# Kernel tuning notes

Hardware: AMD Instinct MI355X
Metric: run time of the kernel (lower is better)

## Reference

```python
import jax, jax.numpy as jnp
import numpy as np
import math

E = 1024      # embed_dim
H = 16        # num_heads
D = E // H    # head_dim = 64 (power of two, padded_dim == head_dim)


def fwht(x):
    """Normalized fast Walsh-Hadamard transform on last dim (power of two)."""
    n = x.shape[-1]
    orig = x.shape
    x = x.reshape(-1, n)
    h = 1
    while h < n:  # log2(n) fixed butterfly stages
        x = x.reshape(-1, n // (2 * h), 2, h)
        a, b = x[:, :, 0, :], x[:, :, 1, :]
        x = jnp.stack([a + b, a - b], axis=2).reshape(-1, n)
        h *= 2
    return (x / math.sqrt(n)).reshape(orig)


def apply_transform(x, diag, alpha, bias):
    # x: [b, h, s, d]; gated FWHT-domain diagonal filter residual
    x_f = fwht(x) * diag
    x_inv = fwht(x_f)
    return x + alpha * x_inv + bias


def setup_inputs() -> dict:
    key = jax.random.key(0)
    ks = jax.random.split(key, 6)
    b, s = 2, 2048
    sc_in = 1.0 / math.sqrt(E)
    return {
        "x": jax.random.normal(ks[0], (b, s, E), jnp.float32),
        "mask": jnp.ones((b, s), jnp.int32),
        "Wqkv": jax.random.normal(ks[1], (E, 3 * E), jnp.float32) * sc_in,
        "bqkv": jnp.zeros((3 * E,), jnp.float32),
        "Wout": jax.random.normal(ks[2], (E, E), jnp.float32) * sc_in,
        "bout": jnp.zeros((E,), jnp.float32),
        "diag": jnp.ones((D,), jnp.float32) * 0.05,
        "alpha": jnp.float32(0.1),
        "bias_h": jnp.zeros((D,), jnp.float32),
    }


def reference(x, mask, Wqkv, bqkv, Wout, bout, diag, alpha, bias_h):
    b, s, _ = x.shape
    qkv = x @ Wqkv + bqkv                       # [b, s, 3E]
    q, k, v = jnp.split(qkv, 3, axis=-1)

    def to_heads(t):
        return t.reshape(b, s, H, D).transpose(0, 2, 1, 3)  # [b, h, s, d]

    qh, kh, vh = to_heads(q), to_heads(k), to_heads(v)
    qh = apply_transform(qh, diag, alpha, bias_h)
    kh = apply_transform(kh, diag, alpha, bias_h)

    scores = jnp.einsum('bhqd,bhkd->bhqk', qh, kh) / math.sqrt(D)
    scores = jnp.where(mask[:, None, None, :] == 0, -jnp.inf, scores)
    weights = jax.nn.softmax(scores, axis=-1)

    out = jnp.einsum('bhqk,bhkd->bhqd', weights, vh)
    out = out.transpose(0, 2, 1, 3).reshape(b, s, E)
    return out @ Wout + bout
```

## Files before the change

kernel.cpp:

```cpp
#include <hip/hip_runtime.h>
#include <hip/hip_bf16.h>
#include <cmath>

#define B_ 2
#define S_ 2048
#define E_ 1024
#define H_ 16
#define M_ (B_*S_)
#define N3_ (3*E_)

typedef unsigned short u16;
typedef unsigned int u32;
typedef __attribute__((ext_vector_type(8))) short bf16x8;
typedef __attribute__((ext_vector_type(8))) _Float16 f16x8;
typedef __attribute__((ext_vector_type(4))) float f32x4;

__device__ __forceinline__ float hw_exp2(float x) {
    return __builtin_amdgcn_exp2f(x);
}
__device__ __forceinline__ u16 cvt_bf(float x) {
    return __builtin_bit_cast(u16, __float2bfloat16(x));
}
__device__ __forceinline__ float bf2f(u16 h) {
    return __uint_as_float((u32)h << 16);
}
__device__ __forceinline__ u16 f2h(float x) {
    _Float16 h = (_Float16)x;
    return __builtin_bit_cast(u16, h);
}
__device__ __forceinline__ float h2f(u16 b) {
    return (float)__builtin_bit_cast(_Float16, b);
}
__device__ __forceinline__ void gld_lds16(const void* g, void* l) {
    __builtin_amdgcn_global_load_lds((const __attribute__((address_space(1))) void*)g,
                                     (__attribute__((address_space(3))) void*)l, 16, 0, 0);
}

template<bool F16>
__device__ __forceinline__ f32x4 mma16(bf16x8 a, bf16x8 b, f32x4 c) {
    if constexpr (F16)
        return __builtin_amdgcn_mfma_f32_16x16x32_f16(
            __builtin_bit_cast(f16x8, a), __builtin_bit_cast(f16x8, b), c, 0, 0, 0);
    else
        return __builtin_amdgcn_mfma_f32_16x16x32_bf16(a, b, c, 0, 0, 0);
}

__global__ __launch_bounds__(256)
void split_a_f16(const float* __restrict__ in, u16* __restrict__ hi, u16* __restrict__ lo, int n4)
{
    int i = blockIdx.x * 256 + threadIdx.x;
    if (i >= n4) return;
    float4 v = ((const float4*)in)[i];
    float vv[4] = {v.x, v.y, v.z, v.w};
    u16 h[4], l[4];
    #pragma unroll
    for (int j = 0; j < 4; j++) {
        h[j] = f2h(vv[j]);
        l[j] = f2h(vv[j] - h2f(h[j]));
    }
    ((uint2*)hi)[i] = make_uint2((u32)h[0] | ((u32)h[1] << 16), (u32)h[2] | ((u32)h[3] << 16));
    ((uint2*)lo)[i] = make_uint2((u32)l[0] | ((u32)l[1] << 16), (u32)l[2] | ((u32)l[3] << 16));
}

__global__ __launch_bounds__(256)
void split_bt_f16hi(const float* __restrict__ W, u16* __restrict__ hi, int K, int N)
{
    __shared__ float tile[64][65];
    const int tid = threadIdx.x;
    const int kb = blockIdx.y * 64, nb = blockIdx.x * 64;
    const int c = tid & 63, r0 = tid >> 6;
    #pragma unroll
    for (int i = 0; i < 16; i++) {
        int r = r0 + i * 4;
        tile[r][c] = W[(size_t)(kb + r) * N + nb + c];
    }
    __syncthreads();
    #pragma unroll
    for (int i = 0; i < 16; i++) {
        int n = r0 + i * 4;
        hi[(size_t)(nb + n) * K + kb + c] = f2h(tile[c][n]);
    }
}

__global__ __launch_bounds__(256)
void split_bt(const float* __restrict__ W, u16* __restrict__ hi, u16* __restrict__ lo,
              int K, int N)
{
    __shared__ float tile[64][65];
    const int tid = threadIdx.x;
    const int kb = blockIdx.y * 64, nb = blockIdx.x * 64;
    const int c = tid & 63, r0 = tid >> 6;
    #pragma unroll
    for (int i = 0; i < 16; i++) {
        int r = r0 + i * 4;
        tile[r][c] = W[(size_t)(kb + r) * N + nb + c];
    }
    __syncthreads();
    #pragma unroll
    for (int i = 0; i < 16; i++) {
        int n = r0 + i * 4;
        float v = tile[c][n];
        u16 h = cvt_bf(v);
        u16 l = cvt_bf(v - bf2f(h));
        size_t o = (size_t)(nb + n) * K + kb + c;
        hi[o] = h; lo[o] = l;
    }
}

template<int NT, bool F16>
__global__ __launch_bounds__(256, 2)
void gemm_t(const u16* __restrict__ Ahi, const u16* __restrict__ Alo,
            const u16* __restrict__ Bhi, const u16* __restrict__ Blo,
            const float* __restrict__ bias, float* __restrict__ C,
            int M, int N, int K)
{
    __shared__ u16 smem[2][(NT + 1) * 4096];
    const int tid = threadIdx.x;
    const int lane = tid & 63;
    const int w = tid >> 6;
    const int wr = w >> 1, wc = w & 1;
    const int l15 = lane & 15, g = lane >> 4;
    const int bm = blockIdx.y * 128;
    const int bn = blockIdx.x * 128;
    const int rsw = ((l15 >> 1) & 3) << 3;
    const f32x4 z4 = {0.f, 0.f, 0.f, 0.f};
    f32x4 acc[4][4];
    #pragma unroll
    for (int m = 0; m < 4; m++)
        #pragma unroll
        for (int n = 0; n < 4; n++) acc[m][n] = z4;

    auto stage = [&](int bi, int ko) {
        #pragma unroll
        for (int ti = 0; ti < NT + 1; ti++) {
            const u16* base = (ti == 0) ? Ahi : (ti == 1) ? Alo : (ti == 2) ? Bhi : Blo;
            const int rb = (ti < 2) ? bm : bn;
            #pragma unroll
            for (int u = 0; u < 2; u++) {
                int c_ = u * 256 + tid;
                int r = c_ >> 2;
                int cs = ((c_ & 3) ^ ((r >> 1) & 3)) << 3;
                gld_lds16(base + (size_t)(rb + r) * K + ko + cs,
                          (char*)&smem[bi][ti * 4096] + ((c_ >> 6) << 10));
            }
        }
    };

    stage(0, 0);
    __syncthreads();
    const int niter = K >> 5;
    for (int i = 0; i < niter; i++) {
        const int cur = i & 1;
        if (i + 1 < niter) stage(cur ^ 1, (i + 1) << 5);
        const u16* sA  = &smem[cur][0];
        const u16* sAl = &smem[cur][4096];
        const u16* sB  = &smem[cur][8192];
        const u16* sBl = &smem[cur][12288];
        bf16x8 ah[4], bh[4], al[4];
        #pragma unroll
        for (int n = 0; n < 4; n++)
            bh[n] = *(const bf16x8*)&sB[(wc*64 + n*16 + l15)*32 + ((g << 3) ^ rsw)];
        #pragma unroll
        for (int m = 0; m < 4; m++)
            ah[m] = *(const bf16x8*)&sA[(wr*64 + m*16 + l15)*32 + ((g << 3) ^ rsw)];
        #pragma unroll
        for (int m = 0; m < 4; m++)
            #pragma unroll
            for (int n = 0; n < 4; n++)
                acc[m][n] = mma16<F16>(ah[m], bh[n], acc[m][n]);
        #pragma unroll
        for (int m = 0; m < 4; m++)
            al[m] = *(const bf16x8*)&sAl[(wr*64 + m*16 + l15)*32 + ((g << 3) ^ rsw)];
        #pragma unroll
        for (int m = 0; m < 4; m++)
            #pragma unroll
            for (int n = 0; n < 4; n++)
                acc[m][n] = mma16<F16>(al[m], bh[n], acc[m][n]);
        if constexpr (NT == 3) {
            bf16x8 bl[4];
            #pragma unroll
            for (int n = 0; n < 4; n++)
                bl[n] = *(const bf16x8*)&sBl[(wc*64 + n*16 + l15)*32 + ((g << 3) ^ rsw)];
            #pragma unroll
            for (int m = 0; m < 4; m++)
                #pragma unroll
                for (int n = 0; n < 4; n++)
                    acc[m][n] = mma16<F16>(ah[m], bl[n], acc[m][n]);
        }
        __syncthreads();
    }
    #pragma unroll
    for (int m = 0; m < 4; m++) {
        #pragma unroll
        for (int n = 0; n < 4; n++) {
            int col = bn + wc*64 + n*16 + l15;
            float bv = bias[col];
            #pragma unroll
            for (int r = 0; r < 4; r++) {
                int row = bm + wr*64 + m*16 + g*4 + r;
                C[(size_t)row * N + col] = acc[m][n][r] + bv;
            }
        }
    }
}

__device__ __forceinline__ float fwht64(float x, int lane)
{
    #pragma unroll
    for (int h = 1; h < 64; h <<= 1) {
        float y = __shfl_xor(x, h, 64);
        x = (lane & h) ? (y - x) : (x + y);
    }
    return x * 0.125f;
}

__global__ __launch_bounds__(256)
void transform_split(const float* __restrict__ qkv, const float* __restrict__ diag,
                     const float* __restrict__ alphap, const float* __restrict__ biasp,
                     u16* __restrict__ qh, u16* __restrict__ kh, u16* __restrict__ vt)
{
    const int lane = threadIdx.x & 63;
    const int w = (blockIdx.x * 256 + threadIdx.x) >> 6;
    const int h = w & (H_ - 1);
    const int s = (w >> 4) & (S_ - 1);
    const int b = w >> 15;
    const int bh = b * H_ + h;
    const float alpha = alphap[0];
    const float dg = diag[lane];
    const float bb = biasp[lane];
    const float* row = qkv + (size_t)(b * S_ + s) * N3_;
    const size_t o = ((size_t)bh * S_ + s) * 64 + lane;

    float xq = row[h*64 + lane];
    float t = fwht64(fwht64(xq, lane) * dg, lane);
    qh[o] = cvt_bf(xq + alpha * t + bb);
    float xk = row[E_ + h*64 + lane];
    t = fwht64(fwht64(xk, lane) * dg, lane);
    kh[o] = cvt_bf(xk + alpha * t + bb);
    vt[((size_t)bh * 64 + lane) * S_ + s] = cvt_bf(row[2*E_ + h*64 + lane]);
}

__global__ __launch_bounds__(256)
void flash_mfma(const u16* __restrict__ qh, const u16* __restrict__ kh,
                const u16* __restrict__ vt, const int* __restrict__ mask,
                u16* __restrict__ ohi, u16* __restrict__ olo)
{
    __shared__ u16 Ks[2][64*64];
    __shared__ u16 Vs[2][64*64];
    __shared__ u16 Ps[4][16*72];
    __shared__ float smask[S_];
    const int tid = threadIdx.x;
    const int lane = tid & 63;
    const int w = tid >> 6;
    const int l15 = lane & 15, g = lane >> 4;
    const int bh = blockIdx.y;
    const int b = bh >> 4, h = bh & 15;
    const int q0 = blockIdx.x * 64;
    const u16* qb = qh + (size_t)bh * S_ * 64;
    const u16* kb = kh + (size_t)bh * S_ * 64;
    const u16* vb = vt + (size_t)bh * 64 * S_;
    const float SCALE2 = 0.18033688011112f;

    #pragma unroll
    for (int i = 0; i < S_/256; i++)
        smask[i*256 + tid] = mask[b*S_ + i*256 + tid] ? 0.f : -3.0e38f;

    bf16x8 qf0, qf1;
    {
        const u16* qr = qb + (size_t)(q0 + w*16 + l15) * 64 + g*8;
        qf0 = *(const bf16x8*)qr;
        qf1 = *(const bf16x8*)(qr + 32);
    }
    const f32x4 z4 = {0.f, 0.f, 0.f, 0.f};
    float m_i = 6.0f, l_i = 0.f;
    f32x4 acc[4];
    #pragma unroll
    for (int n = 0; n < 4; n++) acc[n] = z4;

    const int swz = (l15 & 7) << 3;

    auto stage_kv = [&](int bi, int tt) {
        const int kk0 = tt * 64;
        #pragma unroll
        for (int u = 0; u < 2; u++) {
            int f = u * 256 + tid;
            int r = f >> 3;
            int cs = ((f & 7) ^ (r & 7)) * 8;
            gld_lds16(kb + (size_t)(kk0 + r) * 64 + cs, (char*)&Ks[bi][0] + ((f >> 6) << 10));
            gld_lds16(vb + (size_t)r * S_ + kk0 + cs,   (char*)&Vs[bi][0] + ((f >> 6) << 10));
        }
    };

    stage_kv(0, 0);
    __syncthreads();

    for (int t = 0; t < S_/64; t++) {
        const int cur = t & 1;
        if (t + 1 < S_/64) stage_kv(cur ^ 1, t + 1);
        const int k0 = t * 64;

        f32x4 sv[4];
        __builtin_amdgcn_s_setprio(1);
        #pragma unroll
        for (int nt = 0; nt < 4; nt++) {
            int row = nt*16 + l15;
            bf16x8 ka0 = *(const bf16x8*)&Ks[cur][(row*64 +  0 + g*8) ^ swz];
            bf16x8 ka1 = *(const bf16x8*)&Ks[cur][(row*64 + 32 + g*8) ^ swz];
            sv[nt] = __builtin_amdgcn_mfma_f32_16x16x32_bf16(ka0, qf0, z4, 0, 0, 0);
            sv[nt] = __builtin_amdgcn_mfma_f32_16x16x32_bf16(ka1, qf1, sv[nt], 0, 0, 0);
        }
        __builtin_amdgcn_s_setprio(0);
        #pragma unroll
        for (int nt = 0; nt < 4; nt++) {
            float4 mb = *(const float4*)&smask[k0 + nt*16 + g*4];
            sv[nt][0] = fmaf(sv[nt][0], SCALE2, mb.x);
            sv[nt][1] = fmaf(sv[nt][1], SCALE2, mb.y);
            sv[nt][2] = fmaf(sv[nt][2], SCALE2, mb.z);
            sv[nt][3] = fmaf(sv[nt][3], SCALE2, mb.w);
        }
        float rm = fmaxf(fmaxf(sv[0][0], sv[0][1]), fmaxf(sv[0][2], sv[0][3]));
        #pragma unroll
        for (int nt = 1; nt < 4; nt++) {
            rm = fmaxf(rm, fmaxf(sv[nt][0], sv[nt][1]));
            rm = fmaxf(rm, fmaxf(sv[nt][2], sv[nt][3]));
        }
        rm = fmaxf(rm, __shfl_xor(rm, 16, 64));
        rm = fmaxf(rm, __shfl_xor(rm, 32, 64));
        const int grow = __any(rm > m_i);
        float mn = m_i, fsc = 1.f;
        if (grow) {
            mn = fmaxf(m_i, rm);
            fsc = hw_exp2(m_i - mn);
            m_i = mn;
        }
        float rs = 0.f;
        #pragma unroll
        for (int nt = 0; nt < 4; nt++)
            #pragma unroll
            for (int r = 0; r < 4; r++) {
                float p = hw_exp2(sv[nt][r] - mn);
                sv[nt][r] = p;
                rs += p;
            }
        rs += __shfl_xor(rs, 16, 64);
        rs += __shfl_xor(rs, 32, 64);
        if (grow) {
            l_i = l_i * fsc + rs;
            #pragma unroll
            for (int n = 0; n < 4; n++)
                #pragma unroll
                for (int r = 0; r < 4; r++) acc[n][r] *= fsc;
        } else {
            l_i += rs;
        }
        #pragma unroll
        for (int nt = 0; nt < 4; nt++) {
            u32 p01 = (u32)cvt_bf(sv[nt][0]) | ((u32)cvt_bf(sv[nt][1]) << 16);
            u32 p23 = (u32)cvt_bf(sv[nt][2]) | ((u32)cvt_bf(sv[nt][3]) << 16);
            *(uint2*)&Ps[w][l15*72 + nt*16 + g*4] = make_uint2(p01, p23);
        }
        asm volatile("s_waitcnt lgkmcnt(0)" ::: "memory");
        __builtin_amdgcn_sched_barrier(0);
        __builtin_amdgcn_s_setprio(1);
        #pragma unroll
        for (int kc = 0; kc < 2; kc++) {
            bf16x8 pb = *(const bf16x8*)&Ps[w][l15*72 + kc*32 + g*8];
            #pragma unroll
            for (int nd = 0; nd < 4; nd++) {
                int row = nd*16 + l15;
                bf16x8 vf = *(const bf16x8*)&Vs[cur][(row*64 + kc*32 + g*8) ^ swz];
                acc[nd] = __builtin_amdgcn_mfma_f32_16x16x32_bf16(vf, pb, acc[nd], 0, 0, 0);
            }
        }
        __builtin_amdgcn_s_setprio(0);
        __syncthreads();
    }
    float inv = l_i > 0.f ? 1.f / l_i : 0.f;
    const int q = q0 + w*16 + l15;
    const size_t rowoff = (size_t)(b * S_ + q) * E_ + h*64;
    #pragma unroll
    for (int nd = 0; nd < 4; nd++) {
        #pragma unroll
        for (int r = 0; r < 4; r += 2) {
            float o0 = acc[nd][r]     * inv;
            float o1 = acc[nd][r + 1] * inv;
            u16 h0 = cvt_bf(o0), h1 = cvt_bf(o1);
            u16 lo0 = cvt_bf(o0 - bf2f(h0)), lo1 = cvt_bf(o1 - bf2f(h1));
            int col = nd*16 + g*4 + r;
            *(u32*)&ohi[rowoff + col] = (u32)h0 | ((u32)h1 << 16);
            *(u32*)&olo[rowoff + col] = (u32)lo0 | ((u32)lo1 << 16);
        }
    }
}

extern "C" void kernel_launch(void* const* d_in, const int* in_sizes, int n_in,
                              void* d_out, int out_size, void* d_ws, size_t ws_size,
                              hipStream_t stream)
{
    (void)in_sizes; (void)n_in; (void)out_size; (void)ws_size;
    const float* x     = (const float*)d_in[0];
    const int*   mask  = (const int*)  d_in[1];
    const float* Wqkv  = (const float*)d_in[2];
    const float* bqkv  = (const float*)d_in[3];
    const float* Wout  = (const float*)d_in[4];
    const float* bout  = (const float*)d_in[5];
    const float* diag  = (const float*)d_in[6];
    const float* alpha = (const float*)d_in[7];
    const float* biash = (const float*)d_in[8];
    float* out = (float*)d_out;

    char* ws = (char*)d_ws;
    float* qkv  = (float*)(ws + 0);
    u16* wq_hi  = (u16*)(ws + 50331648);
    u16* qh     = (u16*)(ws + 50331648);
    u16* khp    = (u16*)(ws + 58720256);
    u16* vt     = (u16*)(ws + 67108864);
    u16* x_hi   = (u16*)(ws + 75497472);
    u16* x_lo   = (u16*)(ws + 83886080);
    u16* a_hi   = x_hi;
    u16* a_lo   = x_lo;
    u16* wo_hi  = (u16*)(ws + 92274688);
    u16* wo_lo  = (u16*)(ws + 94371840);

    split_a_f16<<<4096, 256, 0, stream>>>(x, x_hi, x_lo, M_ * E_ / 4);
    split_bt_f16hi<<<dim3(N3_/64, E_/64), 256, 0, stream>>>(Wqkv, wq_hi, E_, N3_);
    split_bt<<<dim3(E_/64, E_/64), 256, 0, stream>>>(Wout, wo_hi, wo_lo, E_, E_);
    gemm_t<2, true><<<dim3(N3_ / 128, M_ / 128), 256, 0, stream>>>(
        x_hi, x_lo, wq_hi, wq_hi, bqkv, qkv, M_, N3_, E_);
    transform_split<<<(B_ * S_ * H_) / 4, 256, 0, stream>>>(
        qkv, diag, alpha, biash, qh, khp, vt);
    flash_mfma<<<dim3(S_ / 64, B_ * H_), 256, 0, stream>>>(
        qh, khp, vt, mask, a_hi, a_lo);
    gemm_t<3, false><<<dim3(E_ / 128, M_ / 128), 256, 0, stream>>>(
        a_hi, a_lo, wo_hi, wo_lo, bout, out, M_, E_, E_);
}
```

Baseline: 308.1 us.

## Keep softmax probabilities in registers for PV MFMA and drop mask LDS

```diff
diff --git a/kernel.cpp b/kernel.cpp
--- a/kernel.cpp
+++ b/kernel.cpp
@@ -12,6 +12,7 @@
 typedef unsigned short u16;
 typedef unsigned int u32;
 typedef __attribute__((ext_vector_type(8))) short bf16x8;
+typedef __attribute__((ext_vector_type(4))) short bf16x4;
 typedef __attribute__((ext_vector_type(8))) _Float16 f16x8;
 typedef __attribute__((ext_vector_type(4))) float f32x4;
 
@@ -60,6 +61,13 @@
     }
     ((uint2*)hi)[i] = make_uint2((u32)h[0] | ((u32)h[1] << 16), (u32)h[2] | ((u32)h[3] << 16));
     ((uint2*)lo)[i] = make_uint2((u32)l[0] | ((u32)l[1] << 16), (u32)l[2] | ((u32)l[3] << 16));
+}
+
+__global__ __launch_bounds__(256)
+void mask2bias(const int* __restrict__ mask, float* __restrict__ mb, int n)
+{
+    int i = blockIdx.x * 256 + threadIdx.x;
+    if (i < n) mb[i] = mask[i] ? 0.f : -3.0e38f;
 }
 
 __global__ __launch_bounds__(256)
@@ -240,30 +248,27 @@
     vt[((size_t)bh * 64 + lane) * S_ + s] = cvt_bf(row[2*E_ + h*64 + lane]);
 }
 
-__global__ __launch_bounds__(256)
+__global__ __launch_bounds__(256, 4)
 void flash_mfma(const u16* __restrict__ qh, const u16* __restrict__ kh,
-                const u16* __restrict__ vt, const int* __restrict__ mask,
+                const u16* __restrict__ vt, const float* __restrict__ mbias,
                 u16* __restrict__ ohi, u16* __restrict__ olo)
 {
     __shared__ u16 Ks[2][64*64];
     __shared__ u16 Vs[2][64*64];
-    __shared__ u16 Ps[4][16*72];
-    __shared__ float smask[S_];
     const int tid = threadIdx.x;
     const int lane = tid & 63;
     const int w = tid >> 6;
     const int l15 = lane & 15, g = lane >> 4;
+    const int g1 = g & 1, gh = g >> 1;
+    const int sx = l15 & 7;
     const int bh = blockIdx.y;
-    const int b = bh >> 4, h = bh & 15;
+    const int b = bh >> 4;
     const int q0 = blockIdx.x * 64;
     const u16* qb = qh + (size_t)bh * S_ * 64;
     const u16* kb = kh + (size_t)bh * S_ * 64;
     const u16* vb = vt + (size_t)bh * 64 * S_;
+    const float* mrow = mbias + b * S_;
     const float SCALE2 = 0.18033688011112f;
-
-    #pragma unroll
-    for (int i = 0; i < S_/256; i++)
-        smask[i*256 + tid] = mask[b*S_ + i*256 + tid] ? 0.f : -3.0e38f;
 
     bf16x8 qf0, qf1;
     {
@@ -277,7 +282,7 @@
     #pragma unroll
     for (int n = 0; n < 4; n++) acc[n] = z4;
 
-    const int swz = (l15 & 7) << 3;
+    const int swz = sx << 3;
 
     auto stage_kv = [&](int bi, int tt) {
         const int kk0 = tt * 64;
@@ -296,8 +301,12 @@
 
     for (int t = 0; t < S_/64; t++) {
         const int cur = t & 1;
+        const int k0 = t * 64;
+        float4 mb[4];
+        #pragma unroll
+        for (int nt = 0; nt < 4; nt++)
+            mb[nt] = *(const float4*)&mrow[k0 + nt*16 + g*4];
         if (t + 1 < S_/64) stage_kv(cur ^ 1, t + 1);
-        const int k0 = t * 64;
 
         f32x4 sv[4];
         __builtin_amdgcn_s_setprio(1);
@@ -312,11 +321,10 @@
         __builtin_amdgcn_s_setprio(0);
         #pragma unroll
         for (int nt = 0; nt < 4; nt++) {
-            float4 mb = *(const float4*)&smask[k0 + nt*16 + g*4];
-            sv[nt][0] = fmaf(sv[nt][0], SCALE2, mb.x);
-            sv[nt][1] = fmaf(sv[nt][1], SCALE2, mb.y);
-            sv[nt][2] = fmaf(sv[nt][2], SCALE2, mb.z);
-            sv[nt][3] = fmaf(sv[nt][3], SCALE2, mb.w);
+            sv[nt][0] = fmaf(sv[nt][0], SCALE2, mb[nt].x);
+            sv[nt][1] = fmaf(sv[nt][1], SCALE2, mb[nt].y);
+            sv[nt][2] = fmaf(sv[nt][2], SCALE2, mb[nt].z);
+            sv[nt][3] = fmaf(sv[nt][3], SCALE2, mb[nt].w);
         }
         float rm = fmaxf(fmaxf(sv[0][0], sv[0][1]), fmaxf(sv[0][2], sv[0][3]));
         #pragma unroll
@@ -353,23 +361,21 @@
         } else {
             l_i += rs;
         }
+        bf16x4 pk[4];
         #pragma unroll
         for (int nt = 0; nt < 4; nt++) {
-            u32 p01 = (u32)cvt_bf(sv[nt][0]) | ((u32)cvt_bf(sv[nt][1]) << 16);
-            u32 p23 = (u32)cvt_bf(sv[nt][2]) | ((u32)cvt_bf(sv[nt][3]) << 16);
-            *(uint2*)&Ps[w][l15*72 + nt*16 + g*4] = make_uint2(p01, p23);
-        }
-        asm volatile("s_waitcnt lgkmcnt(0)" ::: "memory");
-        __builtin_amdgcn_sched_barrier(0);
+            uint2 q2 = make_uint2((u32)cvt_bf(sv[nt][0]) | ((u32)cvt_bf(sv[nt][1]) << 16),
+                                  (u32)cvt_bf(sv[nt][2]) | ((u32)cvt_bf(sv[nt][3]) << 16));
+            pk[nt] = __builtin_bit_cast(bf16x4, q2);
+        }
         __builtin_amdgcn_s_setprio(1);
         #pragma unroll
-        for (int kc = 0; kc < 2; kc++) {
-            bf16x8 pb = *(const bf16x8*)&Ps[w][l15*72 + kc*32 + g*8];
+        for (int kk = 0; kk < 4; kk++) {
             #pragma unroll
             for (int nd = 0; nd < 4; nd++) {
-                int row = nd*16 + l15;
-                bf16x8 vf = *(const bf16x8*)&Vs[cur][(row*64 + kc*32 + g*8) ^ swz];
-                acc[nd] = __builtin_amdgcn_mfma_f32_16x16x32_bf16(vf, pb, acc[nd], 0, 0, 0);
+                int addr = (nd*16 + l15)*64 + ((((kk<<1) + gh) ^ sx) << 3) + g1*4;
+                bf16x4 vf = *(const bf16x4*)&Vs[cur][addr];
+                acc[nd] = __builtin_amdgcn_mfma_f32_16x16x16bf16_1k(vf, pk[kk], acc[nd], 0, 0, 0);
             }
         }
         __builtin_amdgcn_s_setprio(0);
@@ -377,7 +383,7 @@
     }
     float inv = l_i > 0.f ? 1.f / l_i : 0.f;
     const int q = q0 + w*16 + l15;
-    const size_t rowoff = (size_t)(b * S_ + q) * E_ + h*64;
+    const size_t rowoff = (size_t)(b * S_ + q) * E_ + (blockIdx.y & 15)*64;
     #pragma unroll
     for (int nd = 0; nd < 4; nd++) {
         #pragma unroll
@@ -421,16 +427,18 @@
     u16* a_lo   = x_lo;
     u16* wo_hi  = (u16*)(ws + 92274688);
     u16* wo_lo  = (u16*)(ws + 94371840);
+    float* mbias= (float*)(ws + 96468992);
 
     split_a_f16<<<4096, 256, 0, stream>>>(x, x_hi, x_lo, M_ * E_ / 4);
     split_bt_f16hi<<<dim3(N3_/64, E_/64), 256, 0, stream>>>(Wqkv, wq_hi, E_, N3_);
     split_bt<<<dim3(E_/64, E_/64), 256, 0, stream>>>(Wout, wo_hi, wo_lo, E_, E_);
+    mask2bias<<<(B_*S_ + 255)/256, 256, 0, stream>>>(mask, mbias, B_*S_);
     gemm_t<2, true><<<dim3(N3_ / 128, M_ / 128), 256, 0, stream>>>(
         x_hi, x_lo, wq_hi, wq_hi, bqkv, qkv, M_, N3_, E_);
     transform_split<<<(B_ * S_ * H_) / 4, 256, 0, stream>>>(
         qkv, diag, alpha, biash, qh, khp, vt);
     flash_mfma<<<dim3(S_ / 64, B_ * H_), 256, 0, stream>>>(
-        qh, khp, vt, mask, a_hi, a_lo);
+        qh, khp, vt, mbias, a_hi, a_lo);
     gemm_t<3, false><<<dim3(E_ / 128, M_ / 128), 256, 0, stream>>>(
         a_hi, a_lo, wo_hi, wo_lo, bout, out, M_, E_, E_);
 }
```

Measured after the change: 305.2 us. No clear change (-0.9%).
